# Optimization experiments

Hardware: AMD Instinct MI355X
Metric: run time of the kernel (lower is better)

## Reference

```python
import jax, jax.numpy as jnp
import numpy as np

MUL = 32      # multiplicity of each irrep type: 32x0e + 32x1o (dim = 32 + 96 = 128)
NSPEC = 10
NGRAPH = 16
EPS = 1e-5


def _split(x):
    # x: [N, 128] -> scalars [N, 32], vectors [N, 32, 3]
    return x[:, :MUL], x[:, MUL:].reshape(x.shape[0], MUL, 3)


def _cat(s, v):
    return jnp.concatenate([s, v.reshape(v.shape[0], MUL * 3)], axis=1)


def _irreps_linear(s, v, w0, w1, b0=None):
    # e3nn o3.Linear: per-irrep-type multiplicity mixing, /sqrt(fan_in), bias on scalars only
    inv = 1.0 / np.sqrt(MUL)
    s2 = s @ w0 * inv
    if b0 is not None:
        s2 = s2 + b0
    v2 = jnp.einsum('nuc,uw->nwc', v, w1) * inv
    return s2, v2


def _tensor_product(s1, v1, s2, v2, w000, w110, w011, w101):
    # SeparateWeightTensorProduct with per-path internal weights, lmax=1 paths:
    #   0e x 0e -> 0e, 1o x 1o -> 0e (CG = delta/sqrt(3)), 0e x 1o -> 1o, 1o x 0e -> 1o
    inv = 1.0 / np.sqrt(MUL * MUL)
    half = 1.0 / np.sqrt(2.0)  # two paths feed each output irrep
    out0 = (jnp.einsum('nu,nv,uvw->nw', s1, s2, w000)
            + jnp.einsum('nuc,nvc,uvw->nw', v1, v2, w110) / np.sqrt(3.0)) * (inv * half)
    out1 = (jnp.einsum('nu,nvc,uvw->nwc', s1, v2, w011)
            + jnp.einsum('nuc,nv,uvw->nwc', v1, s2, w101)) * (inv * half)
    return out0, out1


def _e3_layer_norm(s, v, batch, ln_w0, ln_b0, ln_w1):
    # per-graph equivariant layer norm: subtract mean on scalars, RMS-normalize each irrep field
    ones = jnp.ones(batch.shape, s.dtype)
    cnt = jnp.maximum(jax.ops.segment_sum(ones, batch, NGRAPH), 1.0)
    mean = jax.ops.segment_sum(s.sum(-1), batch, NGRAPH) / (cnt * MUL)
    s = s - mean[batch][:, None]
    n2s = jax.ops.segment_sum((s * s).sum(-1), batch, NGRAPH) / (cnt * MUL)
    s = s * jax.lax.rsqrt(n2s + EPS)[batch][:, None] * ln_w0 + ln_b0
    n2v = jax.ops.segment_sum((v * v).sum((-1, -2)), batch, NGRAPH) / (cnt * MUL)
    v = v * jax.lax.rsqrt(n2v + EPS)[batch][:, None, None] * ln_w1[None, :, None]
    return s, v


def setup_inputs() -> dict:
    key = jax.random.key(0)
    ks = jax.random.split(key, 24)
    N, B = 50000, 2
    rn = lambda k, sh: jax.random.normal(k, sh, dtype=jnp.float32)
    inp = {
        'node_feats_hidden': rn(ks[0], (B, N, MUL * 4)),
        'node_feats_up': rn(ks[1], (N, MUL * 4)),
        'hl_w0': rn(ks[2], (B, MUL, MUL)), 'hl_w1': rn(ks[3], (B, MUL, MUL)),
        'ul_w0': rn(ks[4], (B, MUL, MUL)), 'ul_w1': rn(ks[5], (B, MUL, MUL)),
        'tp_w000': rn(ks[6], (B, MUL, MUL, MUL)), 'tp_w110': rn(ks[7], (B, MUL, MUL, MUL)),
        'tp_w011': rn(ks[8], (B, MUL, MUL, MUL)), 'tp_w101': rn(ks[9], (B, MUL, MUL, MUL)),
        'lp_w0': rn(ks[10], (B, MUL, MUL)), 'lp_b0': jnp.zeros((B, MUL), jnp.float32),
        'lp_w1': rn(ks[11], (B, MUL, MUL)),
        'sc_w0': rn(ks[12], (B, MUL, NSPEC, MUL)), 'sc_w1': rn(ks[13], (B, MUL, NSPEC, MUL)),
        'ln_w0': jnp.ones((B, MUL), jnp.float32), 'ln_b0': jnp.zeros((B, MUL), jnp.float32),
        'ln_w1': jnp.ones((B, MUL), jnp.float32),
        'sk_w0': rn(ks[14], (B, MUL, MUL)), 'sk_b0': jnp.zeros((B, MUL), jnp.float32),
        'sk_w1': rn(ks[15], (B, MUL, MUL)),
        'node_species': jax.random.randint(ks[16], (N,), 0, NSPEC),
        'batch': jnp.sort(jax.random.randint(ks[17], (N,), 0, NGRAPH)),
    }
    return inp


def reference(node_feats_hidden, node_feats_up, hl_w0, hl_w1, ul_w0, ul_w1,
              tp_w000, tp_w110, tp_w011, tp_w101, lp_w0, lp_b0, lp_w1,
              sc_w0, sc_w1, ln_w0, ln_b0, ln_w1, sk_w0, sk_b0, sk_w1,
              node_species, batch):
    oh = jax.nn.one_hot(node_species, NSPEC, dtype=node_feats_up.dtype)
    inv_sc = 1.0 / np.sqrt(MUL * NSPEC)
    up = node_feats_up
    outs = []
    for b in range(node_feats_hidden.shape[0]):  # num_interactions blocks (fixed, small)
        sh, vh = _split(node_feats_hidden[b])
        su, vu = _split(up)
        shp, vhp = _irreps_linear(sh, vh, hl_w0[b], hl_w1[b])
        sup, vup = _irreps_linear(su, vu, ul_w0[b], ul_w1[b])
        z0, z1 = _tensor_product(shp, vhp, sup, vup,
                                 tp_w000[b], tp_w110[b], tp_w011[b], tp_w101[b])
        z0, z1 = _irreps_linear(z0, z1, lp_w0[b], lp_w1[b], lp_b0[b])
        # self connection: FullyConnectedTensorProduct(hidden, one-hot '10x0e', out)
        z0 = z0 + jnp.einsum('nu,nv,uvw->nw', sh, oh, sc_w0[b]) * inv_sc
        z1 = z1 + jnp.einsum('nuc,nv,uvw->nwc', vh, oh, sc_w1[b]) * inv_sc
        z0, z1 = _e3_layer_norm(z0, z1, batch, ln_w0[b], ln_b0[b], ln_w1[b])
        sk0, sk1 = _irreps_linear(sh, vh, sk_w0[b], sk_w1[b], sk_b0[b])
        out = _cat(z0 + sk0, z1 + sk1)
        outs.append(out)
        up = out  # next block consumes this block's output as node_feats_up
    return jnp.stack(outs)
```

## Files before the change

### kernel.cpp

```cpp
#include <hip/hip_runtime.h>
#include <math.h>

#define MULT 32
#define NSPEC 10
#define NGRAPH 16
#define INV_SC 0.05590169943749474f
#define INV32S 0.17677669529663687f

typedef unsigned short u16;
typedef __bf16 v8bf __attribute__((ext_vector_type(8)));
typedef float v4f __attribute__((ext_vector_type(4)));
typedef unsigned int v4u_t __attribute__((ext_vector_type(4)));

__device__ __forceinline__ u16 f2bf(float f) {
    unsigned int u = __builtin_bit_cast(unsigned int, f);
    unsigned int r = u + 0x7fffu + ((u >> 16) & 1u);
    return (u16)(r >> 16);
}

__device__ __forceinline__ v8bf frag16(const u16* p) {
    return __builtin_bit_cast(v8bf, *(const v4u_t*)p);
}

#define MFMA(a, b, c) __builtin_amdgcn_mfma_f32_16x16x32_bf16(a, b, c, 0, 0, 0)

__global__ void zero_kernel(float* __restrict__ p, int n) {
    int i = blockIdx.x * 256 + threadIdx.x;
    if (i < n) p[i] = 0.0f;
}

__global__ void count_kernel(const int* __restrict__ batch, float* __restrict__ cnt, int N) {
    __shared__ int bins[NGRAPH];
    int t = threadIdx.x;
    if (t < NGRAPH) bins[t] = 0;
    __syncthreads();
    int i = blockIdx.x * 256 + t;
    if (i < N) atomicAdd(&bins[batch[i]], 1);
    __syncthreads();
    if (t < NGRAPH && bins[t] > 0) atomicAdd(&cnt[t], (float)bins[t]);
}

__global__ void stageA_kernel(const float* __restrict__ w000, const float* __restrict__ w110,
                              const float* __restrict__ w011, const float* __restrict__ w101,
                              const float* __restrict__ lp0, const float* __restrict__ lp1,
                              float* __restrict__ tmp1) {
    int gid = blockIdx.x * 256 + threadIdx.x;
    int tslot = gid >> 15;
    int e = gid & 32767;
    int z = e & 31;
    int uv = e >> 5;
    int b = tslot >> 2, path = tslot & 3;
    const float* W = (path == 0 ? w000 : path == 1 ? w110 : path == 2 ? w011 : w101) + b * 32768;
    const float* L = ((path == 0 || path == 1) ? lp0 : lp1) + b * 1024;
    float scale = (path == 1) ? (1.0f / (8192.0f * 1.7320508075688772f)) : (1.0f / 8192.0f);
    const float* wr = W + uv * 32;
    float acc = 0.0f;
    for (int w = 0; w < 32; ++w) acc += wr[w] * L[w * 32 + z];
    tmp1[gid] = acc * scale;
}

__global__ void stageB_kernel(const float* __restrict__ ul0, const float* __restrict__ ul1,
                              const float* __restrict__ tmp1, float* __restrict__ tmp2) {
    int gid = blockIdx.x * 256 + threadIdx.x;
    int tslot = gid >> 15;
    int e = gid & 32767;
    int z = e & 31;
    int bb = (e >> 5) & 31;
    int u = e >> 10;
    int b = tslot >> 2, path = tslot & 3;
    const float* U = ((path == 0 || path == 3) ? ul0 : ul1) + b * 1024;
    const float* in = tmp1 + (size_t)tslot * 32768 + u * 1024 + z;
    float acc = 0.0f;
    for (int v = 0; v < 32; ++v) acc += U[bb * 32 + v] * in[v * 32];
    tmp2[gid] = acc;
}

__global__ void stageC_kernel(const float* __restrict__ hl0, const float* __restrict__ hl1,
                              const float* __restrict__ tmp2, float* __restrict__ Weff) {
    int gid = blockIdx.x * 256 + threadIdx.x;
    int tslot = gid >> 15;
    int e = gid & 32767;
    int z = e & 31;
    int bb = (e >> 5) & 31;
    int a = e >> 10;
    int b = tslot >> 2, path = tslot & 3;
    const float* H = ((path == 0 || path == 2) ? hl0 : hl1) + b * 1024;
    const float* in = tmp2 + (size_t)tslot * 32768 + bb * 32 + z;
    float acc = 0.0f;
    for (int u = 0; u < 32; ++u) acc += H[a * 32 + u] * in[u * 1024];
    Weff[gid] = acc;
}

__global__ void pack_kernel(const float* __restrict__ Weff,
                            const float* __restrict__ sc_w0, const float* __restrict__ sc_w1,
                            u16* __restrict__ packs, int total) {
    int gid = blockIdx.x * 256 + threadIdx.x;
    if (gid >= total) return;
    int b = gid / 151552;
    int e = gid - b * 151552;
    float v;
    if (e < 131072) {
        int which = e >> 15;
        int e2 = e & 32767;
        int k = e2 & 31;
        int z = (e2 >> 5) & 31;
        int hi = e2 >> 10;
        int path = (which == 0) ? 0 : (which == 1) ? 2 : (which == 2) ? 3 : 1;
        int a  = (which < 2) ? k  : hi;
        int bb = (which < 2) ? hi : k;
        v = Weff[(size_t)((b * 4 + path) * 32 + a) * 1024 + bb * 32 + z];
    } else {
        int e2 = e - 131072;
        int which = e2 / 10240;
        int e3 = e2 - which * 10240;
        int s = e3 >> 10, z = (e3 >> 5) & 31, a = e3 & 31;
        const float* S = which ? sc_w1 : sc_w0;
        v = S[(size_t)b * 10240 + a * 320 + s * 32 + z] * INV_SC;
    }
    packs[gid] = f2bf(v);
}

__attribute__((amdgpu_waves_per_eu(4, 4)))
__global__ __launch_bounds__(256)
void tp_kernel(const float* __restrict__ hidden_b, const float* __restrict__ up,
               const u16* __restrict__ pk,
               const float* __restrict__ lp_b0,
               const int* __restrict__ species, const int* __restrict__ batch,
               float* __restrict__ S1, float* __restrict__ S2, float* __restrict__ V2,
               float* __restrict__ zout, int N) {
    constexpr int OFF_000 = 0, OFF_011 = 32768, OFF_101 = 65536, OFF_110 = 98304;
    constexpr int OFF_SC0 = 131072, OFF_SC1 = 141312;

    __shared__ __align__(16) char smem[33792];
    __shared__ int spec_l[16];
    __shared__ int bat_l[16];
    __shared__ float gs1[NGRAPH], gs2[NGRAPH], gv2[NGRAPH];

    u16* sh_bf = (u16*)smem;
    u16* su_bf = (u16*)(smem + 1280);
    u16* vu_bf = (u16*)(smem + 2560);
    u16* vh_bf = (u16*)(smem + 6400);
    float* suT = (float*)(smem + 10240);
    float* vuT = (float*)(smem + 12288);
    float* vhT = (float*)(smem + 18432);
    float* red = (float*)smem;

    const int t = threadIdx.x;
    const int w = t >> 6, lane = t & 63, quad = lane >> 4, c16 = lane & 15;
    const int n0 = blockIdx.x * 16;
    const int nvalid = min(16, N - n0);

    if (t < NGRAPH) { gs1[t] = 0.f; gs2[t] = 0.f; gv2[t] = 0.f; }
    if (t < 16) {
        spec_l[t] = (t < nvalid) ? species[n0 + t] : -1;
        bat_l[t]  = (t < nvalid) ? batch[n0 + t] : 0;
    }
    for (int i = t; i < 2048; i += 256) {
        int n = i >> 7, col = i & 127;
        float hv = 0.f, uv = 0.f;
        if (n < nvalid) {
            hv = hidden_b[(size_t)(n0 + n) * 128 + col];
            uv = up[(size_t)(n0 + n) * 128 + col];
        }
        if (col < 32) {
            sh_bf[n * 40 + col] = f2bf(hv); su_bf[n * 40 + col] = f2bf(uv);
            suT[col * 16 + n] = uv;
        } else {
            int idx = col - 32, c = idx % 3, a = idx / 3;
            vh_bf[(c * 16 + n) * 40 + a] = f2bf(hv);
            vu_bf[(c * 16 + n) * 40 + a] = f2bf(uv);
            vhT[(c * 32 + a) * 16 + n] = hv;
            vuT[(c * 32 + a) * 16 + n] = uv;
        }
    }
    __syncthreads();

    const v4f z4 = {0.f, 0.f, 0.f, 0.f};
    v4f o0[2];
    v4f o1[3][2];
    o0[0] = z4; o0[1] = z4;
#pragma unroll
    for (int c = 0; c < 3; ++c) { o1[c][0] = z4; o1[c][1] = z4; }

    v8bf a_sh = frag16(sh_bf + c16 * 40 + quad * 8);

    {
        const u16* Wb = pk + OFF_000 + (w * 16 * 16 + c16) * 32 + quad * 8;
#pragma unroll 4
        for (int th = 0; th < 8; ++th) {
            int bb = w * 8 + th;
            v4f y = *(const v4f*)(suT + bb * 16 + quad * 4);
            v8bf bf0 = frag16(Wb + (th * 2) * 512);
            v8bf bf1 = frag16(Wb + (th * 2 + 1) * 512);
            v4f C0 = MFMA(a_sh, bf0, z4);
            v4f C1 = MFMA(a_sh, bf1, z4);
#pragma unroll
            for (int r = 0; r < 4; ++r) {
                o0[0][r] += C0[r] * y[r];
                o0[1][r] += C1[r] * y[r];
            }
        }
    }
    {
        const u16* Wb = pk + OFF_011 + (w * 16 * 16 + c16) * 32 + quad * 8;
#pragma unroll 2
        for (int th = 0; th < 8; ++th) {
            int bb = w * 8 + th;
            v8bf bf0 = frag16(Wb + (th * 2) * 512);
            v8bf bf1 = frag16(Wb + (th * 2 + 1) * 512);
            v4f C0 = MFMA(a_sh, bf0, z4);
            v4f C1 = MFMA(a_sh, bf1, z4);
#pragma unroll
            for (int c = 0; c < 3; ++c) {
                v4f y = *(const v4f*)(vuT + (c * 32 + bb) * 16 + quad * 4);
#pragma unroll
                for (int r = 0; r < 4; ++r) {
                    o1[c][0][r] += C0[r] * y[r];
                    o1[c][1][r] += C1[r] * y[r];
                }
            }
        }
    }
    {
        v8bf a_su = frag16(su_bf + c16 * 40 + quad * 8);
        const u16* Wb = pk + OFF_101 + (w * 16 * 16 + c16) * 32 + quad * 8;
#pragma unroll 2
        for (int th = 0; th < 8; ++th) {
            int aa = w * 8 + th;
            v8bf bf0 = frag16(Wb + (th * 2) * 512);
            v8bf bf1 = frag16(Wb + (th * 2 + 1) * 512);
            v4f C0 = MFMA(a_su, bf0, z4);
            v4f C1 = MFMA(a_su, bf1, z4);
#pragma unroll
            for (int c = 0; c < 3; ++c) {
                v4f y = *(const v4f*)(vhT + (c * 32 + aa) * 16 + quad * 4);
#pragma unroll
                for (int r = 0; r < 4; ++r) {
                    o1[c][0][r] += C0[r] * y[r];
                    o1[c][1][r] += C1[r] * y[r];
                }
            }
        }
    }
#pragma unroll
    for (int c = 0; c < 3; ++c) {
        v8bf av = frag16(vu_bf + (c * 16 + c16) * 40 + quad * 8);
        const u16* Wb = pk + OFF_110 + (w * 16 * 16 + c16) * 32 + quad * 8;
#pragma unroll 4
        for (int th = 0; th < 8; ++th) {
            int aa = w * 8 + th;
            v4f y = *(const v4f*)(vhT + (c * 32 + aa) * 16 + quad * 4);
            v8bf bf0 = frag16(Wb + (th * 2) * 512);
            v8bf bf1 = frag16(Wb + (th * 2 + 1) * 512);
            v4f C0 = MFMA(av, bf0, z4);
            v4f C1 = MFMA(av, bf1, z4);
#pragma unroll
            for (int r = 0; r < 4; ++r) {
                o0[0][r] += C0[r] * y[r];
                o0[1][r] += C1[r] * y[r];
            }
        }
    }
    {
        const int s0 = (w < 2) ? w * 3 : 6 + (w - 2) * 2;
        const int ns = (w < 2) ? 3 : 2;
        v8bf zf = __builtin_bit_cast(v8bf, (v4u_t){0u, 0u, 0u, 0u});
        int sp = spec_l[c16];
        for (int si = s0; si < s0 + ns; ++si) {
            bool m = (sp == si);
            v8bf ash_m = m ? a_sh : zf;
#pragma unroll
            for (int zh = 0; zh < 2; ++zh) {
                int boff = (si * 32 + zh * 16 + c16) * 32 + quad * 8;
                v8bf bf0 = frag16(pk + OFF_SC0 + boff);
                v8bf bf1 = frag16(pk + OFF_SC1 + boff);
                o0[zh] = MFMA(ash_m, bf0, o0[zh]);
#pragma unroll
                for (int c = 0; c < 3; ++c) {
                    v8bf av = frag16(vh_bf + (c * 16 + c16) * 40 + quad * 8);
                    v8bf am = m ? av : zf;
                    o1[c][zh] = MFMA(am, bf1, o1[c][zh]);
                }
            }
        }
    }

    __syncthreads();
#pragma unroll
    for (int r = 0; r < 4; ++r) {
        int n = quad * 4 + r;
        float* row = red + (w * 16 + n) * 132;
        row[c16]      = o0[0][r];
        row[16 + c16] = o0[1][r];
#pragma unroll
        for (int c = 0; c < 3; ++c) {
            row[32 + c16 * 3 + c]        = o1[c][0][r];
            row[32 + (16 + c16) * 3 + c] = o1[c][1][r];
        }
    }
    __syncthreads();
    {
        int n = t >> 4, seg = t & 15;
        v4f sa = z4, sb = z4;
#pragma unroll
        for (int ww = 0; ww < 4; ++ww) {
            const float* rp = red + (ww * 16 + n) * 132 + seg * 8;
            sa += *(const v4f*)rp;
            sb += *(const v4f*)(rp + 4);
        }
        float s1p = 0.f, s2p = 0.f, v2p = 0.f;
        if (seg < 4) {
            sa += *(const v4f*)(lp_b0 + seg * 8);
            sb += *(const v4f*)(lp_b0 + seg * 8 + 4);
            s1p = sa[0] + sa[1] + sa[2] + sa[3] + sb[0] + sb[1] + sb[2] + sb[3];
            s2p = sa[0]*sa[0] + sa[1]*sa[1] + sa[2]*sa[2] + sa[3]*sa[3]
                + sb[0]*sb[0] + sb[1]*sb[1] + sb[2]*sb[2] + sb[3]*sb[3];
        } else {
            v2p = sa[0]*sa[0] + sa[1]*sa[1] + sa[2]*sa[2] + sa[3]*sa[3]
                + sb[0]*sb[0] + sb[1]*sb[1] + sb[2]*sb[2] + sb[3]*sb[3];
        }
        if (n < nvalid) {
            float* op = zout + (size_t)(n0 + n) * 128 + seg * 8;
            *(v4f*)op = sa;
            *(v4f*)(op + 4) = sb;
        }
#pragma unroll
        for (int off = 8; off >= 1; off >>= 1) {
            s1p += __shfl_xor(s1p, off, 16);
            s2p += __shfl_xor(s2p, off, 16);
            v2p += __shfl_xor(v2p, off, 16);
        }
        if (seg == 0 && n < nvalid) {
            int g = bat_l[n];
            atomicAdd(&gs1[g], s1p);
            atomicAdd(&gs2[g], s2p);
            atomicAdd(&gv2[g], v2p);
        }
    }
    __syncthreads();
    if (t < NGRAPH) {
        if (gs1[t] != 0.f) atomicAdd(&S1[t], gs1[t]);
        if (gs2[t] != 0.f) atomicAdd(&S2[t], gs2[t]);
        if (gv2[t] != 0.f) atomicAdd(&V2[t], gv2[t]);
    }
}

__global__ __launch_bounds__(256)
void norm_kernel(const float* __restrict__ hidden_b, float* __restrict__ out_b,
                 const float* __restrict__ skw0, const float* __restrict__ skb0,
                 const float* __restrict__ skw1,
                 const float* __restrict__ lnw0, const float* __restrict__ lnb0,
                 const float* __restrict__ lnw1,
                 const int* __restrict__ batch,
                 const float* __restrict__ S1, const float* __restrict__ S2,
                 const float* __restrict__ V2, const float* __restrict__ cnt, int N) {
    __shared__ __align__(16) float sh_l[8][32];
    __shared__ __align__(16) float vh_l[8][96];
    const int t = threadIdx.x, z = t & 31, nl = t >> 5;
    const int n0 = blockIdx.x * 8;
    for (int i = t; i < 8 * 128; i += 256) {
        int n = i >> 7, col = i & 127;
        float v = (n0 + n < N) ? hidden_b[(size_t)(n0 + n) * 128 + col] : 0.f;
        if (col < 32) sh_l[n][col] = v; else vh_l[n][col - 32] = v;
    }
    __syncthreads();
    const int n = n0 + nl;
    if (n >= N) return;

    float sk0 = 0.f, s1 = 0.f, s2 = 0.f, s3 = 0.f;
    for (int a = 0; a < 32; ++a) {
        float w0 = skw0[a * 32 + z];
        float w1 = skw1[a * 32 + z];
        sk0 += sh_l[nl][a] * w0;
        s1 += vh_l[nl][a * 3 + 0] * w1;
        s2 += vh_l[nl][a * 3 + 1] * w1;
        s3 += vh_l[nl][a * 3 + 2] * w1;
    }
    int g = batch[n];
    float cM = fmaxf(cnt[g], 1.0f) * 32.0f;
    float mean = S1[g] / cM;
    float var = fmaxf(S2[g] / cM - mean * mean, 0.0f);
    float rs = rsqrtf(var + 1e-5f);
    float rv = rsqrtf(fmaxf(V2[g] / cM, 0.0f) + 1e-5f);

    size_t base = (size_t)n * 128;
    float z0 = out_b[base + z];
    out_b[base + z] = (z0 - mean) * rs * lnw0[z] + lnb0[z] + sk0 * INV32S + skb0[z];
    float lw = lnw1[z] * rv;
    float x0 = out_b[base + 32 + z * 3 + 0];
    float x1 = out_b[base + 32 + z * 3 + 1];
    float x2 = out_b[base + 32 + z * 3 + 2];
    out_b[base + 32 + z * 3 + 0] = x0 * lw + s1 * INV32S;
    out_b[base + 32 + z * 3 + 1] = x1 * lw + s2 * INV32S;
    out_b[base + 32 + z * 3 + 2] = x2 * lw + s3 * INV32S;
}

extern "C" void kernel_launch(void* const* d_in, const int* in_sizes, int n_in,
                              void* d_out, int out_size, void* d_ws, size_t ws_size,
                              hipStream_t stream) {
    const float* hidden = (const float*)d_in[0];
    const float* up0    = (const float*)d_in[1];
    const float* hl_w0  = (const float*)d_in[2];
    const float* hl_w1  = (const float*)d_in[3];
    const float* ul_w0  = (const float*)d_in[4];
    const float* ul_w1  = (const float*)d_in[5];
    const float* w000   = (const float*)d_in[6];
    const float* w110   = (const float*)d_in[7];
    const float* w011   = (const float*)d_in[8];
    const float* w101   = (const float*)d_in[9];
    const float* lp_w0  = (const float*)d_in[10];
    const float* lp_b0  = (const float*)d_in[11];
    const float* lp_w1  = (const float*)d_in[12];
    const float* sc_w0  = (const float*)d_in[13];
    const float* sc_w1  = (const float*)d_in[14];
    const float* ln_w0  = (const float*)d_in[15];
    const float* ln_b0  = (const float*)d_in[16];
    const float* ln_w1  = (const float*)d_in[17];
    const float* sk_w0  = (const float*)d_in[18];
    const float* sk_b0  = (const float*)d_in[19];
    const float* sk_w1  = (const float*)d_in[20];
    const int* species  = (const int*)d_in[21];
    const int* batch    = (const int*)d_in[22];
    float* out = (float*)d_out;

    const int N = in_sizes[21];
    const int B = in_sizes[0] / (N * 128);

    float* ws = (float*)d_ws;
    float* Weff = ws;
    float* tmp1 = Weff + (size_t)B * 4 * 32768;
    float* tmp2 = tmp1 + (size_t)B * 4 * 32768;
    float* stats = tmp2 + (size_t)B * 4 * 32768;
    float* cnt = stats;
    float* S1 = stats + NGRAPH;
    float* S2 = S1 + B * NGRAPH;
    float* V2 = S2 + B * NGRAPH;
    int statn = NGRAPH + 3 * B * NGRAPH;

    zero_kernel<<<1, 256, 0, stream>>>(stats, statn);
    count_kernel<<<(N + 255) / 256, 256, 0, stream>>>(batch, cnt, N);

    int nb = B * 4 * 32768 / 256;
    stageA_kernel<<<nb, 256, 0, stream>>>(w000, w110, w011, w101, lp_w0, lp_w1, tmp1);
    stageB_kernel<<<nb, 256, 0, stream>>>(ul_w0, ul_w1, tmp1, tmp2);
    stageC_kernel<<<nb, 256, 0, stream>>>(hl_w0, hl_w1, tmp2, Weff);

    u16* packs = (u16*)tmp1;
    int ptotal = B * 151552;
    pack_kernel<<<(ptotal + 255) / 256, 256, 0, stream>>>(Weff, sc_w0, sc_w1, packs, ptotal);

    for (int b = 0; b < B; ++b) {
        const float* up = (b == 0) ? up0 : out + (size_t)(b - 1) * N * 128;
        const u16* pb = packs + (size_t)b * 151552;
        tp_kernel<<<(N + 15) / 16, 256, 0, stream>>>(
            hidden + (size_t)b * N * 128, up, pb,
            lp_b0 + b * MULT, species, batch,
            S1 + b * NGRAPH, S2 + b * NGRAPH, V2 + b * NGRAPH,
            out + (size_t)b * N * 128, N);
        norm_kernel<<<(N + 7) / 8, 256, 0, stream>>>(
            hidden + (size_t)b * N * 128, out + (size_t)b * N * 128,
            sk_w0 + b * 1024, sk_b0 + b * MULT, sk_w1 + b * 1024,
            ln_w0 + b * MULT, ln_b0 + b * MULT, ln_w1 + b * MULT,
            batch, S1 + b * NGRAPH, S2 + b * NGRAPH, V2 + b * NGRAPH, cnt, N);
    }
}
```

Measured before the change: 416.7 us.

## Fuse weight-prep stages into one kernel and shrink tp_kernel LDS use

Result: slower. 729.7 us (+75.1%).

```diff
diff --git a/kernel.cpp b/kernel.cpp
--- a/kernel.cpp
+++ b/kernel.cpp
@@ -40,87 +40,67 @@
     if (t < NGRAPH && bins[t] > 0) atomicAdd(&cnt[t], (float)bins[t]);
 }
 
-__global__ void stageA_kernel(const float* __restrict__ w000, const float* __restrict__ w110,
-                              const float* __restrict__ w011, const float* __restrict__ w101,
-                              const float* __restrict__ lp0, const float* __restrict__ lp1,
-                              float* __restrict__ tmp1) {
-    int gid = blockIdx.x * 256 + threadIdx.x;
-    int tslot = gid >> 15;
-    int e = gid & 32767;
-    int z = e & 31;
-    int uv = e >> 5;
-    int b = tslot >> 2, path = tslot & 3;
-    const float* W = (path == 0 ? w000 : path == 1 ? w110 : path == 2 ? w011 : w101) + b * 32768;
-    const float* L = ((path == 0 || path == 1) ? lp0 : lp1) + b * 1024;
-    float scale = (path == 1) ? (1.0f / (8192.0f * 1.7320508075688772f)) : (1.0f / 8192.0f);
-    const float* wr = W + uv * 32;
-    float acc = 0.0f;
-    for (int w = 0; w < 32; ++w) acc += wr[w] * L[w * 32 + z];
-    tmp1[gid] = acc * scale;
-}
-
-__global__ void stageB_kernel(const float* __restrict__ ul0, const float* __restrict__ ul1,
-                              const float* __restrict__ tmp1, float* __restrict__ tmp2) {
-    int gid = blockIdx.x * 256 + threadIdx.x;
-    int tslot = gid >> 15;
-    int e = gid & 32767;
-    int z = e & 31;
-    int bb = (e >> 5) & 31;
-    int u = e >> 10;
-    int b = tslot >> 2, path = tslot & 3;
-    const float* U = ((path == 0 || path == 3) ? ul0 : ul1) + b * 1024;
-    const float* in = tmp1 + (size_t)tslot * 32768 + u * 1024 + z;
-    float acc = 0.0f;
-    for (int v = 0; v < 32; ++v) acc += U[bb * 32 + v] * in[v * 32];
-    tmp2[gid] = acc;
-}
-
-__global__ void stageC_kernel(const float* __restrict__ hl0, const float* __restrict__ hl1,
-                              const float* __restrict__ tmp2, float* __restrict__ Weff) {
-    int gid = blockIdx.x * 256 + threadIdx.x;
-    int tslot = gid >> 15;
-    int e = gid & 32767;
-    int z = e & 31;
-    int bb = (e >> 5) & 31;
-    int a = e >> 10;
-    int b = tslot >> 2, path = tslot & 3;
-    const float* H = ((path == 0 || path == 2) ? hl0 : hl1) + b * 1024;
-    const float* in = tmp2 + (size_t)tslot * 32768 + bb * 32 + z;
-    float acc = 0.0f;
-    for (int u = 0; u < 32; ++u) acc += H[a * 32 + u] * in[u * 1024];
-    Weff[gid] = acc;
-}
-
-__global__ void pack_kernel(const float* __restrict__ Weff,
-                            const float* __restrict__ sc_w0, const float* __restrict__ sc_w1,
-                            u16* __restrict__ packs, int total) {
-    int gid = blockIdx.x * 256 + threadIdx.x;
-    if (gid >= total) return;
-    int b = gid / 151552;
-    int e = gid - b * 151552;
-    float v;
-    if (e < 131072) {
-        int which = e >> 15;
-        int e2 = e & 32767;
-        int k = e2 & 31;
-        int z = (e2 >> 5) & 31;
-        int hi = e2 >> 10;
-        int path = (which == 0) ? 0 : (which == 1) ? 2 : (which == 2) ? 3 : 1;
-        int a  = (which < 2) ? k  : hi;
-        int bb = (which < 2) ? hi : k;
-        v = Weff[(size_t)((b * 4 + path) * 32 + a) * 1024 + bb * 32 + z];
+__global__ __launch_bounds__(1024)
+void wprep_kernel(const float* __restrict__ w000, const float* __restrict__ w110,
+                  const float* __restrict__ w011, const float* __restrict__ w101,
+                  const float* __restrict__ lp0, const float* __restrict__ lp1,
+                  const float* __restrict__ ul0, const float* __restrict__ ul1,
+                  const float* __restrict__ hl0, const float* __restrict__ hl1,
+                  const float* __restrict__ sc_w0, const float* __restrict__ sc_w1,
+                  u16* __restrict__ packs, int B) {
+    __shared__ float L_lds[1024], U_lds[1024], H_lds[1024], Wu[1024], tmp1[1024];
+    const int blk = blockIdx.x, tid = threadIdx.x;
+    if (blk < B * 4) {
+        const int b = blk >> 2, p = blk & 3;
+        const float* W = (p == 0 ? w000 : p == 1 ? w110 : p == 2 ? w011 : w101) + b * 32768;
+        const float* Lp = ((p == 0 || p == 1) ? lp0 : lp1) + b * 1024;
+        const float* Up = ((p == 0 || p == 3) ? ul0 : ul1) + b * 1024;
+        const float* Hp = ((p == 0 || p == 2) ? hl0 : hl1) + b * 1024;
+        L_lds[tid] = Lp[tid]; U_lds[tid] = Up[tid]; H_lds[tid] = Hp[tid];
+        const float scale = (p == 1) ? (1.0f / (8192.0f * 1.7320508075688772f)) : (1.0f / 8192.0f);
+        const int hi = tid >> 5, z = tid & 31;
+        float acc[32];
+#pragma unroll
+        for (int a = 0; a < 32; ++a) acc[a] = 0.f;
+        __syncthreads();
+        for (int u = 0; u < 32; ++u) {
+            Wu[tid] = W[u * 1024 + tid];
+            __syncthreads();
+            float s = 0.f;
+#pragma unroll
+            for (int ww = 0; ww < 32; ++ww) s += Wu[hi * 32 + ww] * L_lds[ww * 32 + z];
+            tmp1[tid] = s * scale;
+            __syncthreads();
+            float t2 = 0.f;
+#pragma unroll
+            for (int v = 0; v < 32; ++v) t2 += U_lds[hi * 32 + v] * tmp1[v * 32 + z];
+#pragma unroll
+            for (int a = 0; a < 32; ++a) acc[a] += H_lds[a * 32 + u] * t2;
+            __syncthreads();
+        }
+        u16* dst = packs + (size_t)b * 151552;
+#pragma unroll
+        for (int a = 0; a < 32; ++a) {
+            int idx;
+            if (p == 0)      idx = 0     + (hi * 32 + z) * 32 + a;
+            else if (p == 2) idx = 32768 + (hi * 32 + z) * 32 + a;
+            else if (p == 3) idx = 65536 + (a * 32 + z) * 32 + hi;
+            else             idx = 98304 + (a * 32 + z) * 32 + hi;
+            dst[idx] = f2bf(acc[a]);
+        }
     } else {
-        int e2 = e - 131072;
-        int which = e2 / 10240;
-        int e3 = e2 - which * 10240;
-        int s = e3 >> 10, z = (e3 >> 5) & 31, a = e3 & 31;
-        const float* S = which ? sc_w1 : sc_w0;
-        v = S[(size_t)b * 10240 + a * 320 + s * 32 + z] * INV_SC;
-    }
-    packs[gid] = f2bf(v);
-}
-
-__attribute__((amdgpu_waves_per_eu(4, 4)))
+        const int b = blk - B * 4;
+        u16* dst = packs + (size_t)b * 151552 + 131072;
+        for (int e = tid; e < 20480; e += 1024) {
+            int which = e / 10240, e3 = e - which * 10240;
+            int s = e3 >> 10, z = (e3 >> 5) & 31, a = e3 & 31;
+            const float* S = which ? sc_w1 : sc_w0;
+            dst[e] = f2bf(S[(size_t)b * 10240 + a * 320 + s * 32 + z] * INV_SC);
+        }
+    }
+}
+
+__attribute__((amdgpu_waves_per_eu(4, 8)))
 __global__ __launch_bounds__(256)
 void tp_kernel(const float* __restrict__ hidden_b, const float* __restrict__ up,
                const u16* __restrict__ pk,
@@ -131,7 +111,7 @@
     constexpr int OFF_000 = 0, OFF_011 = 32768, OFF_101 = 65536, OFF_110 = 98304;
     constexpr int OFF_SC0 = 131072, OFF_SC1 = 141312;
 
-    __shared__ __align__(16) char smem[33792];
+    __shared__ __align__(16) char smem[24576];
     __shared__ int spec_l[16];
     __shared__ int bat_l[16];
     __shared__ float gs1[NGRAPH], gs2[NGRAPH], gv2[NGRAPH];
@@ -143,7 +123,7 @@
     float* suT = (float*)(smem + 10240);
     float* vuT = (float*)(smem + 12288);
     float* vhT = (float*)(smem + 18432);
-    float* red = (float*)smem;
+    float* zb  = (float*)(smem + 10240);
 
     const int t = threadIdx.x;
     const int w = t >> 6, lane = t & 63, quad = lane >> 4, c16 = lane & 15;
@@ -155,22 +135,28 @@
         spec_l[t] = (t < nvalid) ? species[n0 + t] : -1;
         bat_l[t]  = (t < nvalid) ? batch[n0 + t] : 0;
     }
-    for (int i = t; i < 2048; i += 256) {
-        int n = i >> 7, col = i & 127;
-        float hv = 0.f, uv = 0.f;
+    for (int i = t; i < 512; i += 256) {
+        int n = i >> 5;
+        int q4 = (i & 31) * 4;
+        v4f hv4 = {0.f, 0.f, 0.f, 0.f}, uv4 = {0.f, 0.f, 0.f, 0.f};
         if (n < nvalid) {
-            hv = hidden_b[(size_t)(n0 + n) * 128 + col];
-            uv = up[(size_t)(n0 + n) * 128 + col];
-        }
-        if (col < 32) {
-            sh_bf[n * 40 + col] = f2bf(hv); su_bf[n * 40 + col] = f2bf(uv);
-            suT[col * 16 + n] = uv;
-        } else {
-            int idx = col - 32, c = idx % 3, a = idx / 3;
-            vh_bf[(c * 16 + n) * 40 + a] = f2bf(hv);
-            vu_bf[(c * 16 + n) * 40 + a] = f2bf(uv);
-            vhT[(c * 32 + a) * 16 + n] = hv;
-            vuT[(c * 32 + a) * 16 + n] = uv;
+            hv4 = *(const v4f*)(hidden_b + (size_t)(n0 + n) * 128 + q4);
+            uv4 = *(const v4f*)(up + (size_t)(n0 + n) * 128 + q4);
+        }
+#pragma unroll
+        for (int j = 0; j < 4; ++j) {
+            int col = q4 + j;
+            float hv = hv4[j], uv = uv4[j];
+            if (col < 32) {
+                sh_bf[n * 40 + col] = f2bf(hv); su_bf[n * 40 + col] = f2bf(uv);
+                suT[col * 16 + n] = uv;
+            } else {
+                int idx = col - 32, c = idx % 3, a = idx / 3;
+                vh_bf[(c * 16 + n) * 40 + a] = f2bf(hv);
+                vu_bf[(c * 16 + n) * 40 + a] = f2bf(uv);
+                vhT[(c * 32 + a) * 16 + n] = hv;
+                vuT[(c * 32 + a) * 16 + n] = uv;
+            }
         }
     }
     __syncthreads();
@@ -203,7 +189,7 @@
     }
     {
         const u16* Wb = pk + OFF_011 + (w * 16 * 16 + c16) * 32 + quad * 8;
-#pragma unroll 2
+#pragma unroll 4
         for (int th = 0; th < 8; ++th) {
             int bb = w * 8 + th;
             v8bf bf0 = frag16(Wb + (th * 2) * 512);
@@ -224,7 +210,7 @@
     {
         v8bf a_su = frag16(su_bf + c16 * 40 + quad * 8);
         const u16* Wb = pk + OFF_101 + (w * 16 * 16 + c16) * 32 + quad * 8;
-#pragma unroll 2
+#pragma unroll 4
         for (int th = 0; th < 8; ++th) {
             int aa = w * 8 + th;
             v8bf bf0 = frag16(Wb + (th * 2) * 512);
@@ -286,32 +272,29 @@
     }
 
     __syncthreads();
+    for (int i = t; i < 2048; i += 256) {
+        int col = i & 127;
+        zb[i] = (col < 32) ? lp_b0[col] : 0.f;
+    }
+    __syncthreads();
 #pragma unroll
     for (int r = 0; r < 4; ++r) {
-        int n = quad * 4 + r;
-        float* row = red + (w * 16 + n) * 132;
-        row[c16]      = o0[0][r];
-        row[16 + c16] = o0[1][r];
+        float* zr = zb + (quad * 4 + r) * 128;
+        atomicAdd(zr + c16, o0[0][r]);
+        atomicAdd(zr + 16 + c16, o0[1][r]);
 #pragma unroll
         for (int c = 0; c < 3; ++c) {
-            row[32 + c16 * 3 + c]        = o1[c][0][r];
-            row[32 + (16 + c16) * 3 + c] = o1[c][1][r];
+            atomicAdd(zr + 32 + c16 * 3 + c, o1[c][0][r]);
+            atomicAdd(zr + 32 + (16 + c16) * 3 + c, o1[c][1][r]);
         }
     }
     __syncthreads();
     {
         int n = t >> 4, seg = t & 15;
-        v4f sa = z4, sb = z4;
-#pragma unroll
-        for (int ww = 0; ww < 4; ++ww) {
-            const float* rp = red + (ww * 16 + n) * 132 + seg * 8;
-            sa += *(const v4f*)rp;
-            sb += *(const v4f*)(rp + 4);
-        }
+        v4f sa = *(const v4f*)(zb + n * 128 + seg * 8);
+        v4f sb = *(const v4f*)(zb + n * 128 + seg * 8 + 4);
         float s1p = 0.f, s2p = 0.f, v2p = 0.f;
         if (seg < 4) {
-            sa += *(const v4f*)(lp_b0 + seg * 8);
-            sb += *(const v4f*)(lp_b0 + seg * 8 + 4);
             s1p = sa[0] + sa[1] + sa[2] + sa[3] + sb[0] + sb[1] + sb[2] + sb[3];
             s2p = sa[0]*sa[0] + sa[1]*sa[1] + sa[2]*sa[2] + sa[3]*sa[3]
                 + sb[0]*sb[0] + sb[1]*sb[1] + sb[2]*sb[2] + sb[3]*sb[3];
@@ -358,10 +341,16 @@
     __shared__ __align__(16) float vh_l[8][96];
     const int t = threadIdx.x, z = t & 31, nl = t >> 5;
     const int n0 = blockIdx.x * 8;
-    for (int i = t; i < 8 * 128; i += 256) {
-        int n = i >> 7, col = i & 127;
-        float v = (n0 + n < N) ? hidden_b[(size_t)(n0 + n) * 128 + col] : 0.f;
-        if (col < 32) sh_l[n][col] = v; else vh_l[n][col - 32] = v;
+    for (int i = t; i < 256; i += 256) {
+        int n = i >> 5;
+        int q4 = (i & 31) * 4;
+        v4f v4 = {0.f, 0.f, 0.f, 0.f};
+        if (n0 + n < N) v4 = *(const v4f*)(hidden_b + (size_t)(n0 + n) * 128 + q4);
+#pragma unroll
+        for (int j = 0; j < 4; ++j) {
+            int col = q4 + j;
+            if (col < 32) sh_l[n][col] = v4[j]; else vh_l[n][col - 32] = v4[j];
+        }
     }
     __syncthreads();
     const int n = n0 + nl;
@@ -426,11 +415,9 @@
     const int N = in_sizes[21];
     const int B = in_sizes[0] / (N * 128);
 
-    float* ws = (float*)d_ws;
-    float* Weff = ws;
-    float* tmp1 = Weff + (size_t)B * 4 * 32768;
-    float* tmp2 = tmp1 + (size_t)B * 4 * 32768;
-    float* stats = tmp2 + (size_t)B * 4 * 32768;
+    u16* packs = (u16*)d_ws;
+    size_t pk_bytes = ((size_t)B * 151552 * 2 + 255) & ~(size_t)255;
+    float* stats = (float*)((char*)d_ws + pk_bytes);
     float* cnt = stats;
     float* S1 = stats + NGRAPH;
     float* S2 = S1 + B * NGRAPH;
@@ -439,15 +426,9 @@
 
     zero_kernel<<<1, 256, 0, stream>>>(stats, statn);
     count_kernel<<<(N + 255) / 256, 256, 0, stream>>>(batch, cnt, N);
-
-    int nb = B * 4 * 32768 / 256;
-    stageA_kernel<<<nb, 256, 0, stream>>>(w000, w110, w011, w101, lp_w0, lp_w1, tmp1);
-    stageB_kernel<<<nb, 256, 0, stream>>>(ul_w0, ul_w1, tmp1, tmp2);
-    stageC_kernel<<<nb, 256, 0, stream>>>(hl_w0, hl_w1, tmp2, Weff);
-
-    u16* packs = (u16*)tmp1;
-    int ptotal = B * 151552;
-    pack_kernel<<<(ptotal + 255) / 256, 256, 0, stream>>>(Weff, sc_w0, sc_w1, packs, ptotal);
+    wprep_kernel<<<B * 4 + B, 1024, 0, stream>>>(
+        w000, w110, w011, w101, lp_w0, lp_w1, ul_w0, ul_w1, hl_w0, hl_w1,
+        sc_w0, sc_w1, packs, B);
 
     for (int b = 0; b < B; ++b) {
         const float* up = (b == 0) ? up0 : out + (size_t)(b - 1) * N * 128;
```
